# Kernel tuning notes

Hardware: AMD Instinct MI355X
Metric: run time of the kernel (lower is better)

The kernel has to match this reference:

```python
import jax, jax.numpy as jnp
import numpy as np
import math

D_MODEL = 1024
N_HEAD = 16
D_HEAD = D_MODEL // N_HEAD
SCALE = math.sqrt(D_HEAD)
B, S = 8, 512


def setup_inputs() -> dict:
    key = jax.random.key(0)
    ks = jax.random.split(key, 7)
    x = jax.random.normal(ks[0], (B, S, D_MODEL), dtype=jnp.float32)
    mask = jnp.ones((B, S), dtype=jnp.int32)
    qmask = jax.random.randint(ks[1], (B, S), 0, 2).astype(jnp.int32)
    # params
    Wqkv = jax.random.normal(ks[2], (4 * D_MODEL, D_MODEL), dtype=jnp.float32) / math.sqrt(D_MODEL)
    fc_w = jax.random.normal(ks[3], (D_MODEL, D_MODEL), dtype=jnp.float32) / math.sqrt(D_MODEL)
    fc_b = jnp.zeros((D_MODEL,), dtype=jnp.float32)
    shift = jnp.abs(jax.random.normal(ks[4], (1,), dtype=jnp.float32)) + 0.001
    bias = -jnp.abs(jax.random.normal(ks[5], (1,), dtype=jnp.float32))
    return {"x": x, "mask": mask, "qmask": qmask, "Wqkv": Wqkv,
            "fc_w": fc_w, "fc_b": fc_b, "shift": shift, "bias": bias}


def reference(x, mask, qmask, Wqkv, fc_w, fc_b, shift, bias):
    Bsz, L, D = x.shape
    qkv = x @ Wqkv.T  # [B,S,4D], no bias
    q, k1, k2, v = jnp.split(qkv, 4, axis=-1)

    def heads(t):  # [B,S,D] -> [B,H,S,dh]
        return t.reshape(Bsz, L, N_HEAD, D_HEAD).transpose(0, 2, 1, 3)

    q, k1, k2, v = heads(q), heads(k1), heads(k2), heads(v)

    attn_self = jnp.einsum('bhqd,bhkd->bhqk', q, k1)
    attn_others = jnp.einsum('bhqd,bhkd->bhqk', q, k2)
    same_spk = (qmask[:, :, None] == qmask[:, None, :])[:, None]  # [B,1,S,S]
    attn = jnp.where(same_spk, attn_self, attn_others) / SCALE

    # key padding mask
    attn = jnp.where((mask == 0)[:, None, None, :], -jnp.inf, attn)

    # Gaussian distance bias: -(shift*(i-j)^2 + bias)
    pos = jnp.arange(L, dtype=jnp.float32)
    sq_dist = (pos[:, None] - pos[None, :]) ** 2  # [S,S]
    attn = attn - (shift[0] * sq_dist + bias[0])

    p = jax.nn.softmax(attn, axis=-1)  # dropout=0 (eval)
    out = jnp.einsum('bhqk,bhkd->bhqd', p, v)
    out = out.transpose(0, 2, 1, 3).reshape(Bsz, L, D)
    return out @ fc_w.T + fc_b
```

## Files before the change

### kernel.cpp

```cpp
#include <hip/hip_runtime.h>

typedef unsigned short u16;
typedef __bf16 bf16_t;
typedef bf16_t bf16x8 __attribute__((ext_vector_type(8)));
typedef float f32x4 __attribute__((ext_vector_type(4)));
typedef u16 u16x8 __attribute__((ext_vector_type(8)));
typedef u16 u16x4 __attribute__((ext_vector_type(4)));

__device__ __forceinline__ u16 f2b(float f) {
    unsigned int u = __float_as_uint(f);
    u += 0x7fffu + ((u >> 16) & 1u);
    return (u16)(u >> 16);
}
__device__ __forceinline__ unsigned int pk2(float a, float b) {
    return (unsigned int)f2b(a) | ((unsigned int)f2b(b) << 16);
}

__device__ __forceinline__ f32x4 mfma16(u16x8 a, u16x8 b, f32x4 c) {
    return __builtin_amdgcn_mfma_f32_16x16x32_bf16(
        __builtin_bit_cast(bf16x8, a), __builtin_bit_cast(bf16x8, b), c, 0, 0, 0);
}

#define GLDS16(gp, lp)                                                          \
    __builtin_amdgcn_global_load_lds(                                           \
        (const __attribute__((address_space(1))) void*)(gp),                    \
        (__attribute__((address_space(3))) void*)(lp), 16, 0, 0)

__global__ __launch_bounds__(256) void cvt3_kernel(const float* __restrict__ s0,
                                                   const float* __restrict__ s1,
                                                   const float* __restrict__ s2,
                                                   u16* __restrict__ d0,
                                                   u16* __restrict__ d1,
                                                   u16* __restrict__ d2) {
    int i = (blockIdx.x * 256 + threadIdx.x) * 4;
    const float* src; u16* dst;
    if (i < 4194304)       { src = s0;           dst = d0;           }
    else if (i < 8388608)  { src = s1 - 4194304; dst = d1 - 4194304; }
    else                   { src = s2 - 8388608; dst = d2 - 8388608; }
    float4 f = *(const float4*)(src + i);
    u16x4 o = { f2b(f.x), f2b(f.y), f2b(f.z), f2b(f.w) };
    *(u16x4*)(dst + i) = o;
}

template <int MT, int MODE>
__global__ __launch_bounds__(256) void gemm_bt(
    const u16* __restrict__ A, const u16* __restrict__ Bw,
    u16* __restrict__ Qf, u16* __restrict__ K1f,
    u16* __restrict__ K2f, u16* __restrict__ Vf,
    float* __restrict__ Cf, const float* __restrict__ biasp, int koff)
{
    constexpr int K = 1024;
    constexpr int MF = MT / 32;
    __shared__ u16 As[2][MT * 32];
    __shared__ u16 Bs[2][128 * 32];
    const int t = threadIdx.x;
    const int lane = t & 63;
    const int w = t >> 6;
    const int wm = w >> 1, wn = w & 1;
    const int lr = lane & 15, quad = lane >> 4;

    const int l = blockIdx.x;
    int bx, by;
    if (MODE == 0) {
        by = ((l & 1) | (((l >> 3) & 7) << 1)) + koff;
        bx = ((l >> 1) & 3) | (((l >> 6) & 7) << 2);
    } else {
        by = ((l >> 1) & 3) | (((l >> 5) & 15) << 2);
        bx = (l & 1) | (((l >> 3) & 3) << 1);
    }
    const int tileM = by * MT, tileN = bx * 128;

    f32x4 acc[MF][4] = {};

    const u16* Ag = A + (size_t)(tileM + (t >> 2)) * K + (t & 3) * 8;
    const u16* Bg = Bw + (size_t)(tileN + (t >> 2)) * K + (t & 3) * 8;

    const bool swp = (MODE == 0) && (bx < 24);
    const u16* Afb = swp ? &Bs[0][0] : &As[0][0];
    const u16* Bfb = swp ? &As[0][0] : &Bs[0][0];
    const int AfS = swp ? 128 * 32 : MT * 32;
    const int BfS = swp ? MT * 32 : 128 * 32;

#define STAGE(kk, bufi)                                                         \
    do {                                                                        \
        GLDS16(Ag + (kk), &As[bufi][t * 8]);                                    \
        if (MT == 128) GLDS16(Ag + (kk) + 64 * K, &As[bufi][t * 8 + 2048]);     \
        GLDS16(Bg + (kk), &Bs[bufi][t * 8]);                                    \
        GLDS16(Bg + (kk) + 64 * K, &Bs[bufi][t * 8 + 2048]);                    \
    } while (0)

    STAGE(0, 0);
    __syncthreads();

#pragma unroll 2
    for (int kk = 0; kk < K; kk += 32) {
        const int cur = (kk >> 5) & 1;
        if (kk + 32 < K) STAGE(kk + 32, cur ^ 1);

        u16x8 af[MF], bf[4];
#pragma unroll
        for (int j = 0; j < MF; ++j)
            af[j] = *(const u16x8*)(Afb + cur * AfS + (wm * (MT / 2) + j * 16 + lr) * 32 + quad * 8);
#pragma unroll
        for (int j = 0; j < 4; ++j)
            bf[j] = *(const u16x8*)(Bfb + cur * BfS + (wn * 64 + j * 16 + lr) * 32 + quad * 8);
#pragma unroll
        for (int mi = 0; mi < MF; ++mi)
#pragma unroll
            for (int ni = 0; ni < 4; ++ni)
                acc[mi][ni] = mfma16(af[mi], bf[ni], acc[mi][ni]);

        __syncthreads();
    }
#undef STAGE

    if (MODE == 0) {
        if (swp) {
            const int kvi = bx >> 3;
            const int h = ((bx & 7) << 1) + wm;
            const int bh = ((by >> 2) << 4) + h;
            const int t16b = ((by & 3) << 3) + wn * 4;
            u16* bp = (kvi == 0 ? Qf : (kvi == 1 ? K1f : K2f))
                    + ((size_t)(bh * 32 + t16b) * 2) * 512 + lr * 32 + quad * 4;
#pragma unroll
            for (int mi = 0; mi < MF; ++mi)
#pragma unroll
                for (int ni = 0; ni < 4; ++ni) {
                    uint2 v;
                    v.x = pk2(acc[mi][ni][0], acc[mi][ni][1]);
                    v.y = pk2(acc[mi][ni][2], acc[mi][ni][3]);
                    *(uint2*)(bp + ni * 1024 + (mi >> 1) * 512 + (mi & 1) * 16) = v;
                }
        } else {
            const int h = ((bx - 24) << 1) + wn;
            const int bh = ((by >> 2) << 4) + h;
            const int t5b = ((by & 3) << 2) + wm * 2;
            u16* bp = Vf + ((size_t)(bh * 4) * 16 + t5b) * 512 + lr * 32 + quad * 4;
#pragma unroll
            for (int mi = 0; mi < MF; ++mi)
#pragma unroll
                for (int ni = 0; ni < 4; ++ni) {
                    uint2 v;
                    v.x = pk2(acc[mi][ni][0], acc[mi][ni][1]);
                    v.y = pk2(acc[mi][ni][2], acc[mi][ni][3]);
                    *(uint2*)(bp + ni * 8192 + (mi >> 1) * 512 + (mi & 1) * 16) = v;
                }
        }
    } else {
#pragma unroll
        for (int mi = 0; mi < MF; ++mi)
#pragma unroll
            for (int ni = 0; ni < 4; ++ni) {
                int n = tileN + wn * 64 + ni * 16 + lr;
                float bv = biasp[n];
#pragma unroll
                for (int r = 0; r < 4; ++r) {
                    int m = tileM + wm * (MT / 2) + mi * 16 + quad * 4 + r;
                    Cf[(size_t)m * 1024 + n] = acc[mi][ni][r] + bv;
                }
            }
    }
}

__global__ __launch_bounds__(256) void attn_kernel(
    const u16* __restrict__ qfm, const u16* __restrict__ k1fm,
    const u16* __restrict__ k2fm, const u16* __restrict__ vfm,
    const int* __restrict__ maskp, const int* __restrict__ qmaskp,
    const float* __restrict__ shiftp, const float* __restrict__ biasp,
    u16* __restrict__ ao)
{
    __shared__ u16 Pw[4][2][512];

    const int bh = blockIdx.x & 127, qt = blockIdx.x >> 7;
    const int b = bh >> 4, h = bh & 15;
    const int t = threadIdx.x, lane = t & 63, w = t >> 6;
    const int lr = lane & 15, quad = lane >> 4;
    const float shiftv = shiftp[0], biasv = biasp[0];

    const int qbase = qt * 128 + w * 32;
    const int m16 = qbase >> 4;
    const int loff = lr * 32 + quad * 8;

    const u16* qb = qfm + ((size_t)(bh * 32 + m16) * 2) * 512 + loff;
    u16x8 qa[2][2];
    qa[0][0] = *(const u16x8*)(qb);
    qa[0][1] = *(const u16x8*)(qb + 512);
    qa[1][0] = *(const u16x8*)(qb + 1024);
    qa[1][1] = *(const u16x8*)(qb + 1536);

    int qmr[2][4]; float rowf[2][4];
#pragma unroll
    for (int g = 0; g < 2; ++g)
#pragma unroll
        for (int r = 0; r < 4; ++r) {
            int m = qbase + g * 16 + quad * 4 + r;
            qmr[g][r] = qmaskp[b * 512 + m];
            rowf[g][r] = (float)m;
        }

    f32x4 o[2][4] = {};
    float lsum[2][4] = {};

    u16* pb[2] = { &Pw[w][0][0], &Pw[w][1][0] };
    const int wa0 = quad * 128 + (((lr >> 3) ^ quad) * 8) + (lr & 7);
    const int wa1 = quad * 128 + (((2 | (lr >> 3)) ^ quad) * 8) + (lr & 7);
    const int ra = lr * 32 + ((quad ^ (lr >> 2)) * 8);

    const u16* k1b = k1fm + (size_t)bh * 32768 + loff;
    const u16* k2b = k2fm + (size_t)bh * 32768 + loff;
    const u16* vb  = vfm  + (size_t)bh * 32768 + loff;
    const int* qmb = qmaskp + b * 512;
    const int* kmb = maskp + b * 512;

#pragma unroll 2
    for (int cc = 0; cc < 16; ++cc) {
        const u16* kc1 = k1b + cc * 2048;
        const u16* kc2 = k2b + cc * 2048;
        u16x8 k1f_[2][2], k2f_[2][2];
        k1f_[0][0] = *(const u16x8*)(kc1);
        k1f_[0][1] = *(const u16x8*)(kc1 + 512);
        k1f_[1][0] = *(const u16x8*)(kc1 + 1024);
        k1f_[1][1] = *(const u16x8*)(kc1 + 1536);
        k2f_[0][0] = *(const u16x8*)(kc2);
        k2f_[0][1] = *(const u16x8*)(kc2 + 512);
        k2f_[1][0] = *(const u16x8*)(kc2 + 1024);
        k2f_[1][1] = *(const u16x8*)(kc2 + 1536);
        u16x8 vf_[4];
#pragma unroll
        for (int ot = 0; ot < 4; ++ot)
            vf_[ot] = *(const u16x8*)(vb + (size_t)(ot * 16 + cc) * 512);

        f32x4 z = {0.f, 0.f, 0.f, 0.f};
        f32x4 s1[2][2], s2[2][2];
#pragma unroll
        for (int g = 0; g < 2; ++g)
#pragma unroll
            for (int tg = 0; tg < 2; ++tg) {
                s1[g][tg] = mfma16(qa[g][1], k1f_[tg][1], mfma16(qa[g][0], k1f_[tg][0], z));
                s2[g][tg] = mfma16(qa[g][1], k2f_[tg][1], mfma16(qa[g][0], k2f_[tg][0], z));
            }

        const int col0 = cc * 32 + lr, col1 = col0 + 16;
        const int qmc0 = qmb[col0], qmc1 = qmb[col1];
        const float ka0 = (kmb[col0] ? 0.f : -1e30f) - 10.0f;
        const float ka1 = (kmb[col1] ? 0.f : -1e30f) - 10.0f;
        const float colf0 = (float)col0, colf1 = (float)col1;

#pragma unroll
        for (int g = 0; g < 2; ++g) {
#pragma unroll
            for (int r = 0; r < 4; ++r) {
                float d0 = rowf[g][r] - colf0;
                float d1 = rowf[g][r] - colf1;
                float sel0 = (qmr[g][r] == qmc0) ? s1[g][0][r] : s2[g][0][r];
                float sel1 = (qmr[g][r] == qmc1) ? s1[g][1][r] : s2[g][1][r];
                float v0 = fmaf(sel0, 0.125f, -fmaf(shiftv * d0, d0, biasv)) + ka0;
                float v1 = fmaf(sel1, 0.125f, -fmaf(shiftv * d1, d1, biasv)) + ka1;
                float p0 = __expf(v0);
                float p1 = __expf(v1);
                lsum[g][r] += p0 + p1;
                pb[g][wa0 + r * 32] = f2b(p0);
                pb[g][wa1 + r * 32] = f2b(p1);
            }
        }
#pragma unroll
        for (int g = 0; g < 2; ++g) {
            u16x8 af = *(const u16x8*)(pb[g] + ra);
#pragma unroll
            for (int ot = 0; ot < 4; ++ot)
                o[g][ot] = mfma16(af, vf_[ot], o[g][ot]);
        }
    }

#pragma unroll
    for (int g = 0; g < 2; ++g)
#pragma unroll
        for (int r = 0; r < 4; ++r) {
            float s = lsum[g][r];
#pragma unroll
            for (int m = 1; m < 16; m <<= 1) s += __shfl_xor(s, m);
            float inv = 1.0f / s;
            int grow = b * 512 + qbase + g * 16 + quad * 4 + r;
            u16* orow = ao + (size_t)grow * 1024 + h * 64 + lr;
            orow[0]  = f2b(o[g][0][r] * inv);
            orow[16] = f2b(o[g][1][r] * inv);
            orow[32] = f2b(o[g][2][r] * inv);
            orow[48] = f2b(o[g][3][r] * inv);
        }
}

extern "C" void kernel_launch(void* const* d_in, const int* in_sizes, int n_in,
                              void* d_out, int out_size, void* d_ws, size_t ws_size,
                              hipStream_t stream) {
    (void)in_sizes; (void)n_in; (void)out_size; (void)ws_size;
    const float* x      = (const float*)d_in[0];
    const int*   maskp  = (const int*)d_in[1];
    const int*   qmaskp = (const int*)d_in[2];
    const float* Wqkv   = (const float*)d_in[3];
    const float* fc_w   = (const float*)d_in[4];
    const float* fc_b   = (const float*)d_in[5];
    const float* shiftp = (const float*)d_in[6];
    const float* biasp  = (const float*)d_in[7];
    float* out = (float*)d_out;

    char* ws = (char*)d_ws;
    u16* xb   = (u16*)(ws);
    u16* wb   = (u16*)(ws + (8u << 20));
    u16* fwb  = (u16*)(ws + (16u << 20));
    u16* qfm  = (u16*)(ws + (18u << 20));
    u16* k1fm = (u16*)(ws + (26u << 20));
    u16* k2fm = (u16*)(ws + (34u << 20));
    u16* vfm  = (u16*)(ws + (42u << 20));
    u16* aob  = (u16*)(ws + (50u << 20));

    cvt3_kernel<<<9216, 256, 0, stream>>>(x, Wqkv, fc_w, xb, wb, fwb);
    gemm_bt<128, 0><<<512, 256, 0, stream>>>(xb, wb, qfm, k1fm, k2fm, vfm,
                                             nullptr, nullptr, 0);
    gemm_bt<128, 0><<<512, 256, 0, stream>>>(xb, wb, qfm, k1fm, k2fm, vfm,
                                             nullptr, nullptr, 16);
    attn_kernel<<<512, 256, 0, stream>>>(qfm, k1fm, k2fm, vfm, maskp, qmaskp,
                                         shiftp, biasp, aob);
    gemm_bt<64, 1><<<512, 256, 0, stream>>>(aob, fwb, nullptr, nullptr, nullptr,
                                            nullptr, out, fc_b, 0);
}
```

Baseline: 205.7 us.

## Split-K output GEMM with 128-row tiles and separate bias reduction kernel

The output projection now uses 128x128 tiles with the K dimension split in two halves across 512 blocks. Each block writes fp32 partials in a fragment-contiguous layout, and a new reduction kernel sums the two halves, adds the bias and scatters the result into the output. The two QKV GEMM launches are merged into a single 1024-block launch. The aim is more data reuse per tile and fewer launches, at the cost of an extra 32 MB of partial traffic and one more kernel.

```diff
diff --git a/kernel.cpp b/kernel.cpp
--- a/kernel.cpp
+++ b/kernel.cpp
@@ -47,10 +47,10 @@
     const u16* __restrict__ A, const u16* __restrict__ Bw,
     u16* __restrict__ Qf, u16* __restrict__ K1f,
     u16* __restrict__ K2f, u16* __restrict__ Vf,
-    float* __restrict__ Cf, const float* __restrict__ biasp, int koff)
+    float* __restrict__ Cf)
 {
-    constexpr int K = 1024;
     constexpr int MF = MT / 32;
+    constexpr int KLEN = (MODE == 1) ? 512 : 1024;
     __shared__ u16 As[2][MT * 32];
     __shared__ u16 Bs[2][128 * 32];
     const int t = threadIdx.x;
@@ -60,20 +60,24 @@
     const int lr = lane & 15, quad = lane >> 4;
 
     const int l = blockIdx.x;
-    int bx, by;
+    int bx, by, kh = 0;
     if (MODE == 0) {
-        by = ((l & 1) | (((l >> 3) & 7) << 1)) + koff;
-        bx = ((l >> 1) & 3) | (((l >> 6) & 7) << 2);
+        const int r = l & 511;
+        by = ((r & 1) | (((r >> 3) & 7) << 1)) + ((l >> 9) << 4);
+        bx = ((r >> 1) & 3) | (((r >> 6) & 7) << 2);
     } else {
-        by = ((l >> 1) & 3) | (((l >> 5) & 15) << 2);
-        bx = (l & 1) | (((l >> 3) & 3) << 1);
+        kh = l >> 8;
+        const int r = l & 255;
+        const int xcd = r & 7, i = r >> 3;
+        by = (xcd << 2) | (i & 3);
+        bx = i >> 2;
     }
     const int tileM = by * MT, tileN = bx * 128;
 
     f32x4 acc[MF][4] = {};
 
-    const u16* Ag = A + (size_t)(tileM + (t >> 2)) * K + (t & 3) * 8;
-    const u16* Bg = Bw + (size_t)(tileN + (t >> 2)) * K + (t & 3) * 8;
+    const u16* Ag = A + (size_t)(tileM + (t >> 2)) * 1024 + kh * 512 + (t & 3) * 8;
+    const u16* Bg = Bw + (size_t)(tileN + (t >> 2)) * 1024 + kh * 512 + (t & 3) * 8;
 
     const bool swp = (MODE == 0) && (bx < 24);
     const u16* Afb = swp ? &Bs[0][0] : &As[0][0];
@@ -84,18 +88,18 @@
 #define STAGE(kk, bufi)                                                         \
     do {                                                                        \
         GLDS16(Ag + (kk), &As[bufi][t * 8]);                                    \
-        if (MT == 128) GLDS16(Ag + (kk) + 64 * K, &As[bufi][t * 8 + 2048]);     \
+        if (MT == 128) GLDS16(Ag + (kk) + 64 * 1024, &As[bufi][t * 8 + 2048]);  \
         GLDS16(Bg + (kk), &Bs[bufi][t * 8]);                                    \
-        GLDS16(Bg + (kk) + 64 * K, &Bs[bufi][t * 8 + 2048]);                    \
+        GLDS16(Bg + (kk) + 64 * 1024, &Bs[bufi][t * 8 + 2048]);                 \
     } while (0)
 
     STAGE(0, 0);
     __syncthreads();
 
 #pragma unroll 2
-    for (int kk = 0; kk < K; kk += 32) {
+    for (int kk = 0; kk < KLEN; kk += 32) {
         const int cur = (kk >> 5) & 1;
-        if (kk + 32 < K) STAGE(kk + 32, cur ^ 1);
+        if (kk + 32 < KLEN) STAGE(kk + 32, cur ^ 1);
 
         u16x8 af[MF], bf[4];
 #pragma unroll
@@ -147,19 +151,35 @@
                 }
         }
     } else {
+        float* pbase = Cf + (size_t)kh * 4194304
+                     + (((size_t)((by * 8 + bx) * 4 + w)) * 4096) + lane * 4;
 #pragma unroll
         for (int mi = 0; mi < MF; ++mi)
 #pragma unroll
-            for (int ni = 0; ni < 4; ++ni) {
-                int n = tileN + wn * 64 + ni * 16 + lr;
-                float bv = biasp[n];
-#pragma unroll
-                for (int r = 0; r < 4; ++r) {
-                    int m = tileM + wm * (MT / 2) + mi * 16 + quad * 4 + r;
-                    Cf[(size_t)m * 1024 + n] = acc[mi][ni][r] + bv;
-                }
-            }
+            for (int ni = 0; ni < 4; ++ni)
+                *(f32x4*)(pbase + (mi * 4 + ni) * 256) = acc[mi][ni];
     }
+}
+
+__global__ __launch_bounds__(256) void redk(const float* __restrict__ pk,
+                                            const float* __restrict__ biasp,
+                                            float* __restrict__ out) {
+    int j = blockIdx.x * 256 + threadIdx.x;
+    float4 a = ((const float4*)pk)[j];
+    float4 b = ((const float4*)(pk + 4194304))[j];
+    int chunk = j >> 10, q = j & 1023;
+    int fg = q >> 6, lane = q & 63;
+    int by = chunk >> 5, bx = (chunk >> 2) & 7, w = chunk & 3;
+    int wm = w >> 1, wn = w & 1, mi = fg >> 2, ni = fg & 3;
+    int quad = lane >> 4, lr = lane & 15;
+    int m = by * 128 + wm * 64 + mi * 16 + quad * 4;
+    int n = bx * 128 + wn * 64 + ni * 16 + lr;
+    float bv = biasp[n];
+    float* o = out + (size_t)m * 1024 + n;
+    o[0]    = a.x + b.x + bv;
+    o[1024] = a.y + b.y + bv;
+    o[2048] = a.z + b.z + bv;
+    o[3072] = a.w + b.w + bv;
 }
 
 __global__ __launch_bounds__(256) void attn_kernel(
@@ -304,22 +324,21 @@
     float* out = (float*)d_out;
 
     char* ws = (char*)d_ws;
-    u16* xb   = (u16*)(ws);
-    u16* wb   = (u16*)(ws + (8u << 20));
-    u16* fwb  = (u16*)(ws + (16u << 20));
-    u16* qfm  = (u16*)(ws + (18u << 20));
-    u16* k1fm = (u16*)(ws + (26u << 20));
-    u16* k2fm = (u16*)(ws + (34u << 20));
-    u16* vfm  = (u16*)(ws + (42u << 20));
-    u16* aob  = (u16*)(ws + (50u << 20));
+    u16*   xb   = (u16*)(ws);
+    u16*   wb   = (u16*)(ws + (8u << 20));
+    u16*   fwb  = (u16*)(ws + (16u << 20));
+    u16*   qfm  = (u16*)(ws + (18u << 20));
+    u16*   k1fm = (u16*)(ws + (26u << 20));
+    u16*   k2fm = (u16*)(ws + (34u << 20));
+    u16*   vfm  = (u16*)(ws + (42u << 20));
+    u16*   aob  = (u16*)(ws + (50u << 20));
+    float* pk   = (float*)(ws + (58u << 20));
 
     cvt3_kernel<<<9216, 256, 0, stream>>>(x, Wqkv, fc_w, xb, wb, fwb);
-    gemm_bt<128, 0><<<512, 256, 0, stream>>>(xb, wb, qfm, k1fm, k2fm, vfm,
-                                             nullptr, nullptr, 0);
-    gemm_bt<128, 0><<<512, 256, 0, stream>>>(xb, wb, qfm, k1fm, k2fm, vfm,
-                                             nullptr, nullptr, 16);
+    gemm_bt<128, 0><<<1024, 256, 0, stream>>>(xb, wb, qfm, k1fm, k2fm, vfm, nullptr);
     attn_kernel<<<512, 256, 0, stream>>>(qfm, k1fm, k2fm, vfm, maskp, qmaskp,
                                          shiftp, biasp, aob);
-    gemm_bt<64, 1><<<512, 256, 0, stream>>>(aob, fwb, nullptr, nullptr, nullptr,
-                                            nullptr, out, fc_b, 0);
-}
+    gemm_bt<128, 1><<<512, 256, 0, stream>>>(aob, fwb, nullptr, nullptr, nullptr,
+                                             nullptr, pk);
+    redk<<<4096, 256, 0, stream>>>(pk, fc_b, out);
+}
```

After: 211.1 us. +2.6%, slower.
